# Performance work log

Hardware: AMD Instinct MI355X
Metric: run time of the kernel (lower is better)

The kernel has to match this reference:

```python
import jax, jax.numpy as jnp
import numpy as np

N = 50000      # nodes
E = 800000     # edges (avg degree 16)
IN_DIM = 256
OUT_DIM = 64
HEADS = 4
P_L = 0.1      # freq='low' slope


def setup_inputs() -> dict:
    key = jax.random.key(0)
    ks = jax.random.split(key, 12)
    h = jax.random.normal(ks[0], (N, IN_DIM), dtype=jnp.float32)
    src = jax.random.randint(ks[1], (E,), 0, N, dtype=jnp.int32)
    dst = jax.random.randint(ks[2], (E,), 0, N, dtype=jnp.int32)
    d = jax.random.uniform(ks[3], (N,), dtype=jnp.float32)  # degree norm per node
    s_in = 1.0 / np.sqrt(IN_DIM)
    s_d = 1.0 / np.sqrt(OUT_DIM)
    W_in = jax.random.normal(ks[4], (IN_DIM, HEADS * OUT_DIM), dtype=jnp.float32) * s_in
    b_in = jnp.zeros((HEADS * OUT_DIM,), dtype=jnp.float32)
    W_att = jax.random.normal(ks[5], (HEADS, OUT_DIM, OUT_DIM), dtype=jnp.float32) * s_d
    b_att = jnp.zeros((HEADS, OUT_DIM), dtype=jnp.float32)
    W_g = jax.random.normal(ks[6], (HEADS, 2 * OUT_DIM), dtype=jnp.float32) * s_d
    b_g = jnp.zeros((HEADS,), dtype=jnp.float32)
    W_out = jax.random.normal(ks[7], (HEADS * OUT_DIM, OUT_DIM), dtype=jnp.float32) * s_d
    b_out = jnp.zeros((OUT_DIM,), dtype=jnp.float32)
    return {"h": h, "src": src, "dst": dst, "d": d,
            "W_in": W_in, "b_in": b_in, "W_att": W_att, "b_att": b_att,
            "W_g": W_g, "b_g": b_g, "W_out": W_out, "b_out": b_out}


def reference(h, src, dst, d, W_in, b_in, W_att, b_att, W_g, b_g, W_out, b_out):
    # node transform: [N, H, D]  (dropout is identity in eval mode)
    hh = jax.nn.relu(h @ W_in + b_in).reshape(-1, HEADS, OUT_DIM)
    # per-head att_gate applied at node level (same math as per-edge, cheaper)
    a = jnp.einsum('nhd,hde->nhe', hh, W_att) + b_att           # [N, H, D]
    # gate linear on concat([dst_a, src_a]) split into the two halves of W_g
    g_dst = jnp.einsum('nhd,hd->nh', a, W_g[:, :OUT_DIM])        # [N, H]
    g_src = jnp.einsum('nhd,hd->nh', a, W_g[:, OUT_DIM:])        # [N, H]
    _h = g_dst[dst] + g_src[src] + b_g                           # [E, H]
    # freq='low': relu(where(_h>0, _h, -p_l*_h)) == where(_h>0, _h, -p_l*_h)
    g = jnp.where(_h > 0, _h, -P_L * _h)
    alpha = g * (d[dst] * d[src])[:, None]                       # [E, H]
    msg = hh[src] * alpha[..., None]                             # [E, H, D]
    z = jax.ops.segment_sum(msg, dst, num_segments=N)            # [N, H, D]
    return z.reshape(-1, HEADS * OUT_DIM) @ W_out + b_out        # [N, D]
```

## Files before the change

kernel.cpp:

```cpp
#include <hip/hip_runtime.h>
#include <hip/hip_bf16.h>

#define N_NODES 50000
#define N_EDGES 800000
#define IN_DIM 256
#define OUT_DIM 64
#define HEADS 4
#define HD 256
#define P_L 0.1f
#define TILE_N 64
#define CAP 64
#define OVCAP 4096

typedef __attribute__((ext_vector_type(8))) short bf16x8;
typedef __attribute__((ext_vector_type(4))) float f32x4;

static __device__ __forceinline__ short f2bf(float f) {
    __hip_bfloat16 b = __float2bfloat16(f);
    return *(short*)&b;
}

__global__ __launch_bounds__(256) void prep_kernel(
    const float* __restrict__ W_att, const float* __restrict__ b_att,
    const float* __restrict__ W_g,
    const float* __restrict__ W_in, const float* __restrict__ W_out,
    short* __restrict__ W_bt, short* __restrict__ W_obt2,
    float* __restrict__ v_dst, float* __restrict__ v_src,
    float* __restrict__ c_dst, float* __restrict__ c_src,
    int* __restrict__ cursor, int* __restrict__ ov_count) {
    int b = blockIdx.x, t = threadIdx.x;
    if (b < 256) {
        W_bt[t * 256 + b] = f2bf(W_in[b * 256 + t]);
    } else if (b < 320) {
        int flat = (b - 256) * 256 + t;
        int k = flat & 63, oc = (flat >> 6) & 63, h = flat >> 12;
        W_obt2[flat] = f2bf(W_out[(h * 64 + k) * 64 + oc]);
    } else if (b == 320) {
        int h = t >> 6, dd = t & 63;
        float sd = 0.f, ss = 0.f;
        for (int e = 0; e < 64; ++e) {
            float w = W_att[h * 4096 + dd * 64 + e];
            sd += w * W_g[h * 128 + e];
            ss += w * W_g[h * 128 + 64 + e];
        }
        v_dst[t] = sd;
        v_src[t] = ss;
        if (dd == 0) {
            float cd = 0.f, cs = 0.f;
            for (int e = 0; e < 64; ++e) {
                float bb = b_att[h * 64 + e];
                cd += bb * W_g[h * 128 + e];
                cs += bb * W_g[h * 128 + 64 + e];
            }
            c_dst[h] = cd;
            c_src[h] = cs;
        }
    } else {
        int idx = (b - 321) * 256 + t;
        if (idx < N_NODES) cursor[idx] = 0;
        if (b == 321 && t == 0) *ov_count = 0;
    }
}

__global__ __launch_bounds__(256) void fill_kernel(
    const int* __restrict__ src, const int* __restrict__ dst,
    int* __restrict__ cursor, int* __restrict__ bucket_src,
    int* __restrict__ ov_list, int* __restrict__ ov_count) {
    int e = blockIdx.x * 256 + threadIdx.x;
    if (e >= N_EDGES) return;
    int n = dst[e];
    int pos = atomicAdd(&cursor[n], 1);
    if (pos < CAP) {
        bucket_src[(size_t)n * CAP + pos] = src[e];
    } else {
        int oi = atomicAdd(ov_count, 1);
        if (oi < OVCAP) ov_list[oi] = e;
    }
}

__global__ __launch_bounds__(256, 2) void node_mfma_kernel(
    const float* __restrict__ hin, const short* __restrict__ W_bt,
    const short* __restrict__ W_obt2, const float* __restrict__ b_in,
    const float* __restrict__ v_dst, const float* __restrict__ v_src,
    const float* __restrict__ c_dst, const float* __restrict__ c_src,
    __hip_bfloat16* __restrict__ y, float* __restrict__ gd,
    float* __restrict__ gs) {
    __shared__ short A_lds[TILE_N * 256];
    int t = threadIdx.x;
    int n0 = blockIdx.x * TILE_N;
    bool full = (n0 + TILE_N) <= N_NODES;

    #pragma unroll
    for (int rr = 0; rr < 4; ++rr) {
        int r = rr * 16 + (t >> 4), c0 = (t & 15) * 16;
        int row = n0 + r;
        if (row > N_NODES - 1) row = N_NODES - 1;
        const float* hp = hin + (size_t)row * IN_DIM + c0;
        float fv[16];
        *(float4*)&fv[0]  = *(const float4*)(hp + 0);
        *(float4*)&fv[4]  = *(const float4*)(hp + 4);
        *(float4*)&fv[8]  = *(const float4*)(hp + 8);
        *(float4*)&fv[12] = *(const float4*)(hp + 12);
        short sv[16];
        #pragma unroll
        for (int j = 0; j < 16; ++j) sv[j] = f2bf(fv[j]);
        int swz = (r & 7) << 3;
        int base = r * 256 + c0;
        *(bf16x8*)&A_lds[(base + 0) ^ swz] = *(bf16x8*)&sv[0];
        *(bf16x8*)&A_lds[(base + 8) ^ swz] = *(bf16x8*)&sv[8];
    }
    __syncthreads();

    int l = t & 63, w = t >> 6;
    int lr = l & 15, lg = l >> 4;
    int aswz = (lr & 7) << 3;

    f32x4 acc[4][4];
    #pragma unroll
    for (int rt = 0; rt < 4; ++rt)
        #pragma unroll
        for (int ct = 0; ct < 4; ++ct) acc[rt][ct] = (f32x4){0.f, 0.f, 0.f, 0.f};

    #pragma unroll
    for (int ks = 0; ks < 8; ++ks) {
        bf16x8 bfrag[4], afrag[4];
        #pragma unroll
        for (int ct = 0; ct < 4; ++ct)
            bfrag[ct] = *(const bf16x8*)(W_bt + (size_t)(w * 64 + ct * 16 + lr) * 256 + ks * 32 + lg * 8);
        #pragma unroll
        for (int rt = 0; rt < 4; ++rt)
            afrag[rt] = *(bf16x8*)&A_lds[((rt * 16 + lr) * 256 + ks * 32 + lg * 8) ^ aswz];
        #pragma unroll
        for (int rt = 0; rt < 4; ++rt)
            #pragma unroll
            for (int ct = 0; ct < 4; ++ct)
                acc[rt][ct] = __builtin_amdgcn_mfma_f32_16x16x32_bf16(afrag[rt], bfrag[ct], acc[rt][ct], 0, 0, 0);
    }

    int col[4];
    float vd[4], vs[4], bi[4];
    #pragma unroll
    for (int ct = 0; ct < 4; ++ct) {
        col[ct] = w * 64 + ct * 16 + lr;
        bi[ct] = b_in[col[ct]];
        vd[ct] = v_dst[col[ct]];
        vs[ct] = v_src[col[ct]];
    }
    float pd[4][4], ps[4][4];
    #pragma unroll
    for (int rt = 0; rt < 4; ++rt)
        #pragma unroll
        for (int r = 0; r < 4; ++r) { pd[rt][r] = 0.f; ps[rt][r] = 0.f; }
    #pragma unroll
    for (int rt = 0; rt < 4; ++rt)
        #pragma unroll
        for (int ct = 0; ct < 4; ++ct)
            #pragma unroll
            for (int r = 0; r < 4; ++r) {
                float v = fmaxf(acc[rt][ct][r] + bi[ct], 0.f);
                acc[rt][ct][r] = v;
                pd[rt][r] += v * vd[ct];
                ps[rt][r] += v * vs[ct];
            }
    #pragma unroll
    for (int rt = 0; rt < 4; ++rt)
        #pragma unroll
        for (int r = 0; r < 4; ++r) {
            #pragma unroll
            for (int off = 1; off < 16; off <<= 1) {
                pd[rt][r] += __shfl_xor(pd[rt][r], off, 64);
                ps[rt][r] += __shfl_xor(ps[rt][r], off, 64);
            }
        }
    if (lr == 0) {
        float cd = c_dst[w], cs = c_src[w];
        #pragma unroll
        for (int rt = 0; rt < 4; ++rt)
            #pragma unroll
            for (int r = 0; r < 4; ++r) {
                int m = rt * 16 + lg * 4 + r;
                if (full || (n0 + m) < N_NODES) {
                    gd[(n0 + m) * HEADS + w] = pd[rt][r] + cd;
                    gs[(n0 + m) * HEADS + w] = ps[rt][r] + cs;
                }
            }
    }

    __syncthreads();
    #pragma unroll
    for (int rt = 0; rt < 4; ++rt)
        #pragma unroll
        for (int ct = 0; ct < 4; ++ct)
            #pragma unroll
            for (int r = 0; r < 4; ++r) {
                int m = rt * 16 + lg * 4 + r;
                int idx = m * 256 + col[ct];
                A_lds[idx ^ (((lg * 4 + r) & 7) << 3)] = f2bf(acc[rt][ct][r]);
            }
    __syncthreads();

    f32x4 acc2[4][4];
    #pragma unroll
    for (int rt = 0; rt < 4; ++rt)
        #pragma unroll
        for (int ct = 0; ct < 4; ++ct) acc2[rt][ct] = (f32x4){0.f, 0.f, 0.f, 0.f};
    #pragma unroll
    for (int ks = 0; ks < 2; ++ks) {
        bf16x8 bfrag[4], afrag[4];
        #pragma unroll
        for (int ct = 0; ct < 4; ++ct)
            bfrag[ct] = *(const bf16x8*)(W_obt2 + (size_t)(w * 64 + ct * 16 + lr) * 64 + ks * 32 + lg * 8);
        #pragma unroll
        for (int rt = 0; rt < 4; ++rt)
            afrag[rt] = *(bf16x8*)&A_lds[((rt * 16 + lr) * 256 + w * 64 + ks * 32 + lg * 8) ^ aswz];
        #pragma unroll
        for (int rt = 0; rt < 4; ++rt)
            #pragma unroll
            for (int ct = 0; ct < 4; ++ct)
                acc2[rt][ct] = __builtin_amdgcn_mfma_f32_16x16x32_bf16(afrag[rt], bfrag[ct], acc2[rt][ct], 0, 0, 0);
    }
    #pragma unroll
    for (int rt = 0; rt < 4; ++rt)
        #pragma unroll
        for (int ct = 0; ct < 4; ++ct)
            #pragma unroll
            for (int r = 0; r < 4; ++r) {
                int m = rt * 16 + lg * 4 + r;
                if (full || (n0 + m) < N_NODES)
                    y[(size_t)(n0 + m) * HD + w * 64 + ct * 16 + lr] =
                        __float2bfloat16(acc2[rt][ct][r]);
            }
}

__global__ __launch_bounds__(256) void agg_kernel(
    const int* __restrict__ bucket_src, const int* __restrict__ cursor,
    const int* __restrict__ src, const int* __restrict__ dst,
    const int* __restrict__ ov_list, const int* __restrict__ ov_count,
    const float* __restrict__ dnorm, const float* __restrict__ b_g,
    const __hip_bfloat16* __restrict__ y, const float* __restrict__ gd,
    const float* __restrict__ gs, const float* __restrict__ b_out,
    float* __restrict__ out) {
    int t = threadIdx.x;
    int wv = t >> 6, lane = t & 63;
    int half = lane >> 5, sl = lane & 31;
    int n = blockIdx.x * 8 + wv * 2 + half;
    int head = sl >> 3;
    int deg = cursor[n];
    if (deg > CAP) deg = CAP;
    float dn = dnorm[n];
    float gdh = gd[n * HEADS + head] + b_g[head];
    int degmax = max(deg, __shfl_xor(deg, 32, 64));

    const uint4* yb = (const uint4*)y;
    const int* bp = bucket_src + (size_t)n * CAP;
    float a[8];
    #pragma unroll
    for (int j = 0; j < 8; ++j) a[j] = 0.f;

    for (int i = 0; i < degmax; i += 8) {
        int sarr[8];
        #pragma unroll
        for (int j = 0; j < 8; ++j) {
            int e = i + j;
            sarr[j] = (e < deg) ? bp[e] : -1;
        }
        float gsv[8], dnv[8];
        uint4 v[8];
        #pragma unroll
        for (int j = 0; j < 8; ++j) {
            int s = sarr[j] < 0 ? 0 : sarr[j];
            gsv[j] = gs[s * HEADS + head];
            dnv[j] = dnorm[s];
            v[j] = yb[(size_t)s * 32 + sl];
        }
        #pragma unroll
        for (int j = 0; j < 8; ++j) {
            float _h = gdh + gsv[j];
            float g = _h > 0.f ? _h : -P_L * _h;
            float al = (sarr[j] < 0) ? 0.f : g * dn * dnv[j];
            a[0] += __uint_as_float(v[j].x << 16) * al;
            a[1] += __uint_as_float(v[j].x & 0xffff0000u) * al;
            a[2] += __uint_as_float(v[j].y << 16) * al;
            a[3] += __uint_as_float(v[j].y & 0xffff0000u) * al;
            a[4] += __uint_as_float(v[j].z << 16) * al;
            a[5] += __uint_as_float(v[j].z & 0xffff0000u) * al;
            a[6] += __uint_as_float(v[j].w << 16) * al;
            a[7] += __uint_as_float(v[j].w & 0xffff0000u) * al;
        }
    }

    int cnt = *ov_count;
    if (cnt > 0) {
        if (cnt > OVCAP) cnt = OVCAP;
        for (int j = 0; j < cnt; ++j) {
            int e = ov_list[j];
            if (dst[e] == n) {
                int s = src[e];
                float _h = gdh + gs[s * HEADS + head];
                float g = _h > 0.f ? _h : -P_L * _h;
                float al = g * dn * dnorm[s];
                uint4 vv = yb[(size_t)s * 32 + sl];
                a[0] += __uint_as_float(vv.x << 16) * al;
                a[1] += __uint_as_float(vv.x & 0xffff0000u) * al;
                a[2] += __uint_as_float(vv.y << 16) * al;
                a[3] += __uint_as_float(vv.y & 0xffff0000u) * al;
                a[4] += __uint_as_float(vv.z << 16) * al;
                a[5] += __uint_as_float(vv.z & 0xffff0000u) * al;
                a[6] += __uint_as_float(vv.w << 16) * al;
                a[7] += __uint_as_float(vv.w & 0xffff0000u) * al;
            }
        }
    }

    #pragma unroll
    for (int j = 0; j < 8; ++j) {
        a[j] += __shfl_xor(a[j], 8, 64);
        a[j] += __shfl_xor(a[j], 16, 64);
    }
    if (sl < 8) {
        float4 b0 = *(const float4*)&b_out[sl * 8];
        float4 b1 = *(const float4*)&b_out[sl * 8 + 4];
        float4 o0, o1;
        o0.x = a[0] + b0.x; o0.y = a[1] + b0.y; o0.z = a[2] + b0.z; o0.w = a[3] + b0.w;
        o1.x = a[4] + b1.x; o1.y = a[5] + b1.y; o1.z = a[6] + b1.z; o1.w = a[7] + b1.w;
        *(float4*)&out[(size_t)n * OUT_DIM + sl * 8] = o0;
        *(float4*)&out[(size_t)n * OUT_DIM + sl * 8 + 4] = o1;
    }
}

extern "C" void kernel_launch(void* const* d_in, const int* in_sizes, int n_in,
                              void* d_out, int out_size, void* d_ws, size_t ws_size,
                              hipStream_t stream) {
    const float* h     = (const float*)d_in[0];
    const int*   src   = (const int*)d_in[1];
    const int*   dst   = (const int*)d_in[2];
    const float* dnorm = (const float*)d_in[3];
    const float* W_in  = (const float*)d_in[4];
    const float* b_in  = (const float*)d_in[5];
    const float* W_att = (const float*)d_in[6];
    const float* b_att = (const float*)d_in[7];
    const float* W_g   = (const float*)d_in[8];
    const float* b_g   = (const float*)d_in[9];
    const float* W_out = (const float*)d_in[10];
    const float* b_out = (const float*)d_in[11];
    float* out = (float*)d_out;

    char* ws = (char*)d_ws;
    __hip_bfloat16* y = (__hip_bfloat16*)ws;
    ws += (size_t)N_NODES * HD * sizeof(__hip_bfloat16);
    float* gd     = (float*)ws;  ws += (size_t)N_NODES * HEADS * sizeof(float);
    float* gs     = (float*)ws;  ws += (size_t)N_NODES * HEADS * sizeof(float);
    float* v_dst  = (float*)ws;  ws += 256 * sizeof(float);
    float* v_src  = (float*)ws;  ws += 256 * sizeof(float);
    float* c_dst  = (float*)ws;  ws += 16;
    float* c_src  = (float*)ws;  ws += 16;
    int* cursor     = (int*)ws;  ws += (size_t)N_NODES * sizeof(int);
    int* ov_count   = (int*)ws;  ws += 16;
    int* ov_list    = (int*)ws;  ws += OVCAP * sizeof(int);
    int* bucket_src = (int*)ws;  ws += (size_t)N_NODES * CAP * sizeof(int);
    short* W_bt     = (short*)ws; ws += 256 * 256 * sizeof(short);
    short* W_obt2   = (short*)ws;

    prep_kernel<<<517, 256, 0, stream>>>(W_att, b_att, W_g, W_in, W_out,
                                         W_bt, W_obt2, v_dst, v_src, c_dst, c_src,
                                         cursor, ov_count);
    fill_kernel<<<(N_EDGES + 255) / 256, 256, 0, stream>>>(src, dst, cursor, bucket_src,
                                                           ov_list, ov_count);
    node_mfma_kernel<<<(N_NODES + TILE_N - 1) / TILE_N, 256, 0, stream>>>(
        h, W_bt, W_obt2, b_in, v_dst, v_src, c_dst, c_src, y, gd, gs);
    agg_kernel<<<N_NODES / 8, 256, 0, stream>>>(bucket_src, cursor, src, dst,
                                                ov_list, ov_count, dnorm, b_g,
                                                y, gd, gs, b_out, out);
}
```

Measured before the change: 160.2 us.

## Merge prep and fill kernels; use 8-wave blocks in node MFMA kernel

Zeroing of the bucket cursor and overflow counter moves to hipMemsetAsync calls, so the edge bucket-fill blocks can join the weight-prep kernel in a single launch. The node MFMA kernel now runs 512 threads per block, with each wave covering 32 rows and one head instead of 64 rows, which halves the accumulator registers per wave and gives each block more waves. The goal is fewer kernel launches and better latency hiding in the node transform. In exchange it adds two memset launches, and the larger block drops the min-2-blocks occupancy hint.

New measurement: 180.4 us. 1.13x slower.

```diff
diff --git a/kernel.cpp b/kernel.cpp
--- a/kernel.cpp
+++ b/kernel.cpp
@@ -11,6 +11,7 @@
 #define TILE_N 64
 #define CAP 64
 #define OVCAP 4096
+#define FILL_OFF 321
 
 typedef __attribute__((ext_vector_type(8))) short bf16x8;
 typedef __attribute__((ext_vector_type(4))) float f32x4;
@@ -20,22 +21,38 @@
     return *(short*)&b;
 }
 
-__global__ __launch_bounds__(256) void prep_kernel(
+__global__ __launch_bounds__(256) void prep_fill_kernel(
     const float* __restrict__ W_att, const float* __restrict__ b_att,
     const float* __restrict__ W_g,
     const float* __restrict__ W_in, const float* __restrict__ W_out,
+    const int* __restrict__ src, const int* __restrict__ dst,
     short* __restrict__ W_bt, short* __restrict__ W_obt2,
     float* __restrict__ v_dst, float* __restrict__ v_src,
     float* __restrict__ c_dst, float* __restrict__ c_src,
-    int* __restrict__ cursor, int* __restrict__ ov_count) {
+    int* __restrict__ cursor, int* __restrict__ bucket_src,
+    int* __restrict__ ov_list, int* __restrict__ ov_count) {
     int b = blockIdx.x, t = threadIdx.x;
+    if (b >= FILL_OFF) {
+        int e = (b - FILL_OFF) * 256 + t;
+        if (e < N_EDGES) {
+            int n = dst[e];
+            int pos = atomicAdd(&cursor[n], 1);
+            if (pos < CAP) {
+                bucket_src[(size_t)n * CAP + pos] = src[e];
+            } else {
+                int oi = atomicAdd(ov_count, 1);
+                if (oi < OVCAP) ov_list[oi] = e;
+            }
+        }
+        return;
+    }
     if (b < 256) {
         W_bt[t * 256 + b] = f2bf(W_in[b * 256 + t]);
     } else if (b < 320) {
         int flat = (b - 256) * 256 + t;
         int k = flat & 63, oc = (flat >> 6) & 63, h = flat >> 12;
         W_obt2[flat] = f2bf(W_out[(h * 64 + k) * 64 + oc]);
-    } else if (b == 320) {
+    } else {
         int h = t >> 6, dd = t & 63;
         float sd = 0.f, ss = 0.f;
         for (int e = 0; e < 64; ++e) {
@@ -55,30 +72,10 @@
             c_dst[h] = cd;
             c_src[h] = cs;
         }
-    } else {
-        int idx = (b - 321) * 256 + t;
-        if (idx < N_NODES) cursor[idx] = 0;
-        if (b == 321 && t == 0) *ov_count = 0;
-    }
-}
-
-__global__ __launch_bounds__(256) void fill_kernel(
-    const int* __restrict__ src, const int* __restrict__ dst,
-    int* __restrict__ cursor, int* __restrict__ bucket_src,
-    int* __restrict__ ov_list, int* __restrict__ ov_count) {
-    int e = blockIdx.x * 256 + threadIdx.x;
-    if (e >= N_EDGES) return;
-    int n = dst[e];
-    int pos = atomicAdd(&cursor[n], 1);
-    if (pos < CAP) {
-        bucket_src[(size_t)n * CAP + pos] = src[e];
-    } else {
-        int oi = atomicAdd(ov_count, 1);
-        if (oi < OVCAP) ov_list[oi] = e;
-    }
-}
-
-__global__ __launch_bounds__(256, 2) void node_mfma_kernel(
+    }
+}
+
+__global__ __launch_bounds__(512) void node_mfma_kernel(
     const float* __restrict__ hin, const short* __restrict__ W_bt,
     const short* __restrict__ W_obt2, const float* __restrict__ b_in,
     const float* __restrict__ v_dst, const float* __restrict__ v_src,
@@ -91,8 +88,8 @@
     bool full = (n0 + TILE_N) <= N_NODES;
 
     #pragma unroll
-    for (int rr = 0; rr < 4; ++rr) {
-        int r = rr * 16 + (t >> 4), c0 = (t & 15) * 16;
+    for (int rr = 0; rr < 2; ++rr) {
+        int r = rr * 32 + (t >> 4), c0 = (t & 15) * 16;
         int row = n0 + r;
         if (row > N_NODES - 1) row = N_NODES - 1;
         const float* hp = hin + (size_t)row * IN_DIM + c0;
@@ -111,124 +108,125 @@
     }
     __syncthreads();
 
-    int l = t & 63, w = t >> 6;
+    int l = t & 63, w8 = t >> 6;
+    int rp = w8 >> 2, hd = w8 & 3;
     int lr = l & 15, lg = l >> 4;
     int aswz = (lr & 7) << 3;
 
-    f32x4 acc[4][4];
-    #pragma unroll
-    for (int rt = 0; rt < 4; ++rt)
-        #pragma unroll
-        for (int ct = 0; ct < 4; ++ct) acc[rt][ct] = (f32x4){0.f, 0.f, 0.f, 0.f};
+    f32x4 acc[2][4];
+    #pragma unroll
+    for (int i = 0; i < 2; ++i)
+        #pragma unroll
+        for (int ct = 0; ct < 4; ++ct) acc[i][ct] = (f32x4){0.f, 0.f, 0.f, 0.f};
 
     #pragma unroll
     for (int ks = 0; ks < 8; ++ks) {
-        bf16x8 bfrag[4], afrag[4];
-        #pragma unroll
-        for (int ct = 0; ct < 4; ++ct)
-            bfrag[ct] = *(const bf16x8*)(W_bt + (size_t)(w * 64 + ct * 16 + lr) * 256 + ks * 32 + lg * 8);
-        #pragma unroll
-        for (int rt = 0; rt < 4; ++rt)
-            afrag[rt] = *(bf16x8*)&A_lds[((rt * 16 + lr) * 256 + ks * 32 + lg * 8) ^ aswz];
-        #pragma unroll
-        for (int rt = 0; rt < 4; ++rt)
+        bf16x8 bfrag[4], afrag[2];
+        #pragma unroll
+        for (int ct = 0; ct < 4; ++ct)
+            bfrag[ct] = *(const bf16x8*)(W_bt + (size_t)(hd * 64 + ct * 16 + lr) * 256 + ks * 32 + lg * 8);
+        #pragma unroll
+        for (int i = 0; i < 2; ++i)
+            afrag[i] = *(bf16x8*)&A_lds[((rp * 32 + i * 16 + lr) * 256 + ks * 32 + lg * 8) ^ aswz];
+        #pragma unroll
+        for (int i = 0; i < 2; ++i)
             #pragma unroll
             for (int ct = 0; ct < 4; ++ct)
-                acc[rt][ct] = __builtin_amdgcn_mfma_f32_16x16x32_bf16(afrag[rt], bfrag[ct], acc[rt][ct], 0, 0, 0);
+                acc[i][ct] = __builtin_amdgcn_mfma_f32_16x16x32_bf16(afrag[i], bfrag[ct], acc[i][ct], 0, 0, 0);
     }
 
     int col[4];
     float vd[4], vs[4], bi[4];
     #pragma unroll
     for (int ct = 0; ct < 4; ++ct) {
-        col[ct] = w * 64 + ct * 16 + lr;
+        col[ct] = hd * 64 + ct * 16 + lr;
         bi[ct] = b_in[col[ct]];
         vd[ct] = v_dst[col[ct]];
         vs[ct] = v_src[col[ct]];
     }
-    float pd[4][4], ps[4][4];
-    #pragma unroll
-    for (int rt = 0; rt < 4; ++rt)
-        #pragma unroll
-        for (int r = 0; r < 4; ++r) { pd[rt][r] = 0.f; ps[rt][r] = 0.f; }
-    #pragma unroll
-    for (int rt = 0; rt < 4; ++rt)
+    float pd[2][4], ps[2][4];
+    #pragma unroll
+    for (int i = 0; i < 2; ++i)
+        #pragma unroll
+        for (int r = 0; r < 4; ++r) { pd[i][r] = 0.f; ps[i][r] = 0.f; }
+    #pragma unroll
+    for (int i = 0; i < 2; ++i)
         #pragma unroll
         for (int ct = 0; ct < 4; ++ct)
             #pragma unroll
             for (int r = 0; r < 4; ++r) {
-                float v = fmaxf(acc[rt][ct][r] + bi[ct], 0.f);
-                acc[rt][ct][r] = v;
-                pd[rt][r] += v * vd[ct];
-                ps[rt][r] += v * vs[ct];
-            }
-    #pragma unroll
-    for (int rt = 0; rt < 4; ++rt)
+                float v = fmaxf(acc[i][ct][r] + bi[ct], 0.f);
+                acc[i][ct][r] = v;
+                pd[i][r] += v * vd[ct];
+                ps[i][r] += v * vs[ct];
+            }
+    #pragma unroll
+    for (int i = 0; i < 2; ++i)
         #pragma unroll
         for (int r = 0; r < 4; ++r) {
             #pragma unroll
             for (int off = 1; off < 16; off <<= 1) {
-                pd[rt][r] += __shfl_xor(pd[rt][r], off, 64);
-                ps[rt][r] += __shfl_xor(ps[rt][r], off, 64);
+                pd[i][r] += __shfl_xor(pd[i][r], off, 64);
+                ps[i][r] += __shfl_xor(ps[i][r], off, 64);
             }
         }
     if (lr == 0) {
-        float cd = c_dst[w], cs = c_src[w];
-        #pragma unroll
-        for (int rt = 0; rt < 4; ++rt)
+        float cd = c_dst[hd], cs = c_src[hd];
+        #pragma unroll
+        for (int i = 0; i < 2; ++i)
             #pragma unroll
             for (int r = 0; r < 4; ++r) {
-                int m = rt * 16 + lg * 4 + r;
+                int m = rp * 32 + i * 16 + lg * 4 + r;
                 if (full || (n0 + m) < N_NODES) {
-                    gd[(n0 + m) * HEADS + w] = pd[rt][r] + cd;
-                    gs[(n0 + m) * HEADS + w] = ps[rt][r] + cs;
+                    gd[(n0 + m) * HEADS + hd] = pd[i][r] + cd;
+                    gs[(n0 + m) * HEADS + hd] = ps[i][r] + cs;
                 }
             }
     }
 
     __syncthreads();
     #pragma unroll
-    for (int rt = 0; rt < 4; ++rt)
+    for (int i = 0; i < 2; ++i)
         #pragma unroll
         for (int ct = 0; ct < 4; ++ct)
             #pragma unroll
             for (int r = 0; r < 4; ++r) {
-                int m = rt * 16 + lg * 4 + r;
+                int m = rp * 32 + i * 16 + lg * 4 + r;
                 int idx = m * 256 + col[ct];
-                A_lds[idx ^ (((lg * 4 + r) & 7) << 3)] = f2bf(acc[rt][ct][r]);
+                A_lds[idx ^ ((m & 7) << 3)] = f2bf(acc[i][ct][r]);
             }
     __syncthreads();
 
-    f32x4 acc2[4][4];
-    #pragma unroll
-    for (int rt = 0; rt < 4; ++rt)
-        #pragma unroll
-        for (int ct = 0; ct < 4; ++ct) acc2[rt][ct] = (f32x4){0.f, 0.f, 0.f, 0.f};
+    f32x4 acc2[2][4];
+    #pragma unroll
+    for (int i = 0; i < 2; ++i)
+        #pragma unroll
+        for (int ct = 0; ct < 4; ++ct) acc2[i][ct] = (f32x4){0.f, 0.f, 0.f, 0.f};
     #pragma unroll
     for (int ks = 0; ks < 2; ++ks) {
-        bf16x8 bfrag[4], afrag[4];
-        #pragma unroll
-        for (int ct = 0; ct < 4; ++ct)
-            bfrag[ct] = *(const bf16x8*)(W_obt2 + (size_t)(w * 64 + ct * 16 + lr) * 64 + ks * 32 + lg * 8);
-        #pragma unroll
-        for (int rt = 0; rt < 4; ++rt)
-            afrag[rt] = *(bf16x8*)&A_lds[((rt * 16 + lr) * 256 + w * 64 + ks * 32 + lg * 8) ^ aswz];
-        #pragma unroll
-        for (int rt = 0; rt < 4; ++rt)
+        bf16x8 bfrag[4], afrag[2];
+        #pragma unroll
+        for (int ct = 0; ct < 4; ++ct)
+            bfrag[ct] = *(const bf16x8*)(W_obt2 + (size_t)(hd * 64 + ct * 16 + lr) * 64 + ks * 32 + lg * 8);
+        #pragma unroll
+        for (int i = 0; i < 2; ++i)
+            afrag[i] = *(bf16x8*)&A_lds[((rp * 32 + i * 16 + lr) * 256 + hd * 64 + ks * 32 + lg * 8) ^ aswz];
+        #pragma unroll
+        for (int i = 0; i < 2; ++i)
             #pragma unroll
             for (int ct = 0; ct < 4; ++ct)
-                acc2[rt][ct] = __builtin_amdgcn_mfma_f32_16x16x32_bf16(afrag[rt], bfrag[ct], acc2[rt][ct], 0, 0, 0);
-    }
-    #pragma unroll
-    for (int rt = 0; rt < 4; ++rt)
+                acc2[i][ct] = __builtin_amdgcn_mfma_f32_16x16x32_bf16(afrag[i], bfrag[ct], acc2[i][ct], 0, 0, 0);
+    }
+    #pragma unroll
+    for (int i = 0; i < 2; ++i)
         #pragma unroll
         for (int ct = 0; ct < 4; ++ct)
             #pragma unroll
             for (int r = 0; r < 4; ++r) {
-                int m = rt * 16 + lg * 4 + r;
+                int m = rp * 32 + i * 16 + lg * 4 + r;
                 if (full || (n0 + m) < N_NODES)
-                    y[(size_t)(n0 + m) * HD + w * 64 + ct * 16 + lr] =
-                        __float2bfloat16(acc2[rt][ct][r]);
+                    y[(size_t)(n0 + m) * HD + hd * 64 + ct * 16 + lr] =
+                        __float2bfloat16(acc2[i][ct][r]);
             }
 }
 
@@ -361,12 +359,14 @@
     short* W_bt     = (short*)ws; ws += 256 * 256 * sizeof(short);
     short* W_obt2   = (short*)ws;
 
-    prep_kernel<<<517, 256, 0, stream>>>(W_att, b_att, W_g, W_in, W_out,
-                                         W_bt, W_obt2, v_dst, v_src, c_dst, c_src,
-                                         cursor, ov_count);
-    fill_kernel<<<(N_EDGES + 255) / 256, 256, 0, stream>>>(src, dst, cursor, bucket_src,
-                                                           ov_list, ov_count);
-    node_mfma_kernel<<<(N_NODES + TILE_N - 1) / TILE_N, 256, 0, stream>>>(
+    hipMemsetAsync(cursor, 0, (size_t)N_NODES * sizeof(int), stream);
+    hipMemsetAsync(ov_count, 0, sizeof(int), stream);
+
+    prep_fill_kernel<<<FILL_OFF + (N_EDGES + 255) / 256, 256, 0, stream>>>(
+        W_att, b_att, W_g, W_in, W_out, src, dst,
+        W_bt, W_obt2, v_dst, v_src, c_dst, c_src,
+        cursor, bucket_src, ov_list, ov_count);
+    node_mfma_kernel<<<(N_NODES + TILE_N - 1) / TILE_N, 512, 0, stream>>>(
         h, W_bt, W_obt2, b_in, v_dst, v_src, c_dst, c_src, y, gd, gs);
     agg_kernel<<<N_NODES / 8, 256, 0, stream>>>(bucket_src, cursor, src, dst,
                                                 ov_list, ov_count, dnorm, b_g,
```

## Split node MFMA kernel across 8 waves with LDS partial-gate reduction

Applied to the files above, without the earlier changes.

Node transform kernel now runs 512 threads per block, splitting each head's 64 output columns between two waves so each wave holds half the accumulators. Partial gate dot products from the two waves are reduced through new shared arrays before writing gd/gs, and the second GEMM likewise splits its output columns. This aims to raise wave-level parallelism and latency hiding per block and lower register pressure, at the cost of an extra LDS reduction and duplicated A-fragment LDS reads per wave pair.

Result: no change. 160.3 us, median of 2 (+0.0%).

```diff
diff --git a/kernel.cpp b/kernel.cpp
--- a/kernel.cpp
+++ b/kernel.cpp
@@ -78,7 +78,7 @@
     }
 }
 
-__global__ __launch_bounds__(256, 2) void node_mfma_kernel(
+__global__ __launch_bounds__(512) void node_mfma_kernel(
     const float* __restrict__ hin, const short* __restrict__ W_bt,
     const short* __restrict__ W_obt2, const float* __restrict__ b_in,
     const float* __restrict__ v_dst, const float* __restrict__ v_src,
@@ -86,13 +86,15 @@
     __hip_bfloat16* __restrict__ y, float* __restrict__ gd,
     float* __restrict__ gs) {
     __shared__ short A_lds[TILE_N * 256];
+    __shared__ float sm_pd[8][TILE_N];
+    __shared__ float sm_ps[8][TILE_N];
     int t = threadIdx.x;
     int n0 = blockIdx.x * TILE_N;
     bool full = (n0 + TILE_N) <= N_NODES;
 
     #pragma unroll
-    for (int rr = 0; rr < 4; ++rr) {
-        int r = rr * 16 + (t >> 4), c0 = (t & 15) * 16;
+    for (int rr = 0; rr < 2; ++rr) {
+        int r = rr * 32 + (t >> 4), c0 = (t & 15) * 16;
         int row = n0 + r;
         if (row > N_NODES - 1) row = N_NODES - 1;
         const float* hp = hin + (size_t)row * IN_DIM + c0;
@@ -111,40 +113,43 @@
     }
     __syncthreads();
 
-    int l = t & 63, w = t >> 6;
+    int l = t & 63, w8 = t >> 6;
+    int hd = w8 & 3, ch = w8 >> 2;
     int lr = l & 15, lg = l >> 4;
     int aswz = (lr & 7) << 3;
 
-    f32x4 acc[4][4];
-    #pragma unroll
-    for (int rt = 0; rt < 4; ++rt)
-        #pragma unroll
-        for (int ct = 0; ct < 4; ++ct) acc[rt][ct] = (f32x4){0.f, 0.f, 0.f, 0.f};
+    f32x4 acc[4][2];
+    #pragma unroll
+    for (int rt = 0; rt < 4; ++rt)
+        #pragma unroll
+        for (int c = 0; c < 2; ++c) acc[rt][c] = (f32x4){0.f, 0.f, 0.f, 0.f};
+
+    int col[2];
+    #pragma unroll
+    for (int c = 0; c < 2; ++c) col[c] = hd * 64 + (ch * 2 + c) * 16 + lr;
 
     #pragma unroll
     for (int ks = 0; ks < 8; ++ks) {
-        bf16x8 bfrag[4], afrag[4];
-        #pragma unroll
-        for (int ct = 0; ct < 4; ++ct)
-            bfrag[ct] = *(const bf16x8*)(W_bt + (size_t)(w * 64 + ct * 16 + lr) * 256 + ks * 32 + lg * 8);
+        bf16x8 bfrag[2], afrag[4];
+        #pragma unroll
+        for (int c = 0; c < 2; ++c)
+            bfrag[c] = *(const bf16x8*)(W_bt + (size_t)col[c] * 256 + ks * 32 + lg * 8);
         #pragma unroll
         for (int rt = 0; rt < 4; ++rt)
             afrag[rt] = *(bf16x8*)&A_lds[((rt * 16 + lr) * 256 + ks * 32 + lg * 8) ^ aswz];
         #pragma unroll
         for (int rt = 0; rt < 4; ++rt)
             #pragma unroll
-            for (int ct = 0; ct < 4; ++ct)
-                acc[rt][ct] = __builtin_amdgcn_mfma_f32_16x16x32_bf16(afrag[rt], bfrag[ct], acc[rt][ct], 0, 0, 0);
-    }
-
-    int col[4];
-    float vd[4], vs[4], bi[4];
-    #pragma unroll
-    for (int ct = 0; ct < 4; ++ct) {
-        col[ct] = w * 64 + ct * 16 + lr;
-        bi[ct] = b_in[col[ct]];
-        vd[ct] = v_dst[col[ct]];
-        vs[ct] = v_src[col[ct]];
+            for (int c = 0; c < 2; ++c)
+                acc[rt][c] = __builtin_amdgcn_mfma_f32_16x16x32_bf16(afrag[rt], bfrag[c], acc[rt][c], 0, 0, 0);
+    }
+
+    float vd[2], vs[2], bi[2];
+    #pragma unroll
+    for (int c = 0; c < 2; ++c) {
+        bi[c] = b_in[col[c]];
+        vd[c] = v_dst[col[c]];
+        vs[c] = v_src[col[c]];
     }
     float pd[4][4], ps[4][4];
     #pragma unroll
@@ -154,13 +159,13 @@
     #pragma unroll
     for (int rt = 0; rt < 4; ++rt)
         #pragma unroll
-        for (int ct = 0; ct < 4; ++ct)
+        for (int c = 0; c < 2; ++c)
             #pragma unroll
             for (int r = 0; r < 4; ++r) {
-                float v = fmaxf(acc[rt][ct][r] + bi[ct], 0.f);
-                acc[rt][ct][r] = v;
-                pd[rt][r] += v * vd[ct];
-                ps[rt][r] += v * vs[ct];
+                float v = fmaxf(acc[rt][c][r] + bi[c], 0.f);
+                acc[rt][c][r] = v;
+                pd[rt][r] += v * vd[c];
+                ps[rt][r] += v * vs[c];
             }
     #pragma unroll
     for (int rt = 0; rt < 4; ++rt)
@@ -173,16 +178,13 @@
             }
         }
     if (lr == 0) {
-        float cd = c_dst[w], cs = c_src[w];
         #pragma unroll
         for (int rt = 0; rt < 4; ++rt)
             #pragma unroll
             for (int r = 0; r < 4; ++r) {
                 int m = rt * 16 + lg * 4 + r;
-                if (full || (n0 + m) < N_NODES) {
-                    gd[(n0 + m) * HEADS + w] = pd[rt][r] + cd;
-                    gs[(n0 + m) * HEADS + w] = ps[rt][r] + cs;
-                }
+                sm_pd[w8][m] = pd[rt][r];
+                sm_ps[w8][m] = ps[rt][r];
             }
     }
 
@@ -190,45 +192,53 @@
     #pragma unroll
     for (int rt = 0; rt < 4; ++rt)
         #pragma unroll
-        for (int ct = 0; ct < 4; ++ct)
+        for (int c = 0; c < 2; ++c)
             #pragma unroll
             for (int r = 0; r < 4; ++r) {
                 int m = rt * 16 + lg * 4 + r;
-                int idx = m * 256 + col[ct];
-                A_lds[idx ^ (((lg * 4 + r) & 7) << 3)] = f2bf(acc[rt][ct][r]);
+                int idx = m * 256 + col[c];
+                A_lds[idx ^ ((m & 7) << 3)] = f2bf(acc[rt][c][r]);
             }
     __syncthreads();
 
-    f32x4 acc2[4][4];
-    #pragma unroll
-    for (int rt = 0; rt < 4; ++rt)
-        #pragma unroll
-        for (int ct = 0; ct < 4; ++ct) acc2[rt][ct] = (f32x4){0.f, 0.f, 0.f, 0.f};
+    if (t < 256) {
+        int m = t & 63, hh = t >> 6;
+        if (full || (n0 + m) < N_NODES) {
+            gd[(n0 + m) * HEADS + hh] = sm_pd[hh][m] + sm_pd[hh + 4][m] + c_dst[hh];
+            gs[(n0 + m) * HEADS + hh] = sm_ps[hh][m] + sm_ps[hh + 4][m] + c_src[hh];
+        }
+    }
+
+    f32x4 acc2[4][2];
+    #pragma unroll
+    for (int rt = 0; rt < 4; ++rt)
+        #pragma unroll
+        for (int c = 0; c < 2; ++c) acc2[rt][c] = (f32x4){0.f, 0.f, 0.f, 0.f};
     #pragma unroll
     for (int ks = 0; ks < 2; ++ks) {
-        bf16x8 bfrag[4], afrag[4];
-        #pragma unroll
-        for (int ct = 0; ct < 4; ++ct)
-            bfrag[ct] = *(const bf16x8*)(W_obt2 + (size_t)(w * 64 + ct * 16 + lr) * 64 + ks * 32 + lg * 8);
-        #pragma unroll
-        for (int rt = 0; rt < 4; ++rt)
-            afrag[rt] = *(bf16x8*)&A_lds[((rt * 16 + lr) * 256 + w * 64 + ks * 32 + lg * 8) ^ aswz];
-        #pragma unroll
-        for (int rt = 0; rt < 4; ++rt)
-            #pragma unroll
-            for (int ct = 0; ct < 4; ++ct)
-                acc2[rt][ct] = __builtin_amdgcn_mfma_f32_16x16x32_bf16(afrag[rt], bfrag[ct], acc2[rt][ct], 0, 0, 0);
-    }
-    #pragma unroll
-    for (int rt = 0; rt < 4; ++rt)
-        #pragma unroll
-        for (int ct = 0; ct < 4; ++ct)
+        bf16x8 bfrag[2], afrag[4];
+        #pragma unroll
+        for (int c = 0; c < 2; ++c)
+            bfrag[c] = *(const bf16x8*)(W_obt2 + (size_t)col[c] * 64 + ks * 32 + lg * 8);
+        #pragma unroll
+        for (int rt = 0; rt < 4; ++rt)
+            afrag[rt] = *(bf16x8*)&A_lds[((rt * 16 + lr) * 256 + hd * 64 + ks * 32 + lg * 8) ^ aswz];
+        #pragma unroll
+        for (int rt = 0; rt < 4; ++rt)
+            #pragma unroll
+            for (int c = 0; c < 2; ++c)
+                acc2[rt][c] = __builtin_amdgcn_mfma_f32_16x16x32_bf16(afrag[rt], bfrag[c], acc2[rt][c], 0, 0, 0);
+    }
+    #pragma unroll
+    for (int rt = 0; rt < 4; ++rt)
+        #pragma unroll
+        for (int c = 0; c < 2; ++c)
             #pragma unroll
             for (int r = 0; r < 4; ++r) {
                 int m = rt * 16 + lg * 4 + r;
                 if (full || (n0 + m) < N_NODES)
-                    y[(size_t)(n0 + m) * HD + w * 64 + ct * 16 + lr] =
-                        __float2bfloat16(acc2[rt][ct][r]);
+                    y[(size_t)(n0 + m) * HD + col[c]] =
+                        __float2bfloat16(acc2[rt][c][r]);
             }
 }
 
@@ -366,7 +376,7 @@
                                          cursor, ov_count);
     fill_kernel<<<(N_EDGES + 255) / 256, 256, 0, stream>>>(src, dst, cursor, bucket_src,
                                                            ov_list, ov_count);
-    node_mfma_kernel<<<(N_NODES + TILE_N - 1) / TILE_N, 256, 0, stream>>>(
+    node_mfma_kernel<<<(N_NODES + TILE_N - 1) / TILE_N, 512, 0, stream>>>(
         h, W_bt, W_obt2, b_in, v_dst, v_src, c_dst, c_src, y, gd, gs);
     agg_kernel<<<N_NODES / 8, 256, 0, stream>>>(bucket_src, cursor, src, dst,
                                                 ov_list, ov_count, dnorm, b_g,
```
